# Kernel optimization log

Measured on AMD Instinct MI355X. Metric: run time of the kernel, lower is better.

Reference implementation:

```python
import jax, jax.numpy as jnp
from jax import lax
import numpy as np

EPS_BN = 1e-5


def _bn(x, g, b, axis):
    # eval-mode BatchNorm with running_mean=0, running_var=1
    shape = [1] * x.ndim
    shape[axis] = -1
    scale = (g / jnp.sqrt(1.0 + EPS_BN)).reshape(shape)
    return x * scale + b.reshape(shape)


def farthest_point_sample(xyz, npoint):
    B, N, _ = xyz.shape
    bidx = jnp.arange(B)

    def body(carry, _):
        dist, far = carry                      # [B,N], [B]
        centroid = xyz[bidx, far]              # [B,3]
        d = jnp.sum((xyz - centroid[:, None, :]) ** 2, axis=-1)
        dist = jnp.minimum(dist, d)
        return (dist, jnp.argmax(dist, axis=-1)), far

    init = (jnp.full((B, N), 1e10, xyz.dtype), jnp.zeros((B,), jnp.int32))
    _, idxs = lax.scan(body, init, None, length=npoint)
    return idxs.T                              # [B,npoint]


def square_distance(src, dst):
    # [B,S,3] x [B,N,3] -> [B,S,N]
    d = -2.0 * jnp.einsum('bsc,bnc->bsn', src, dst)
    d = d + jnp.sum(src ** 2, -1)[:, :, None] + jnp.sum(dst ** 2, -1)[:, None, :]
    return d


def sample_and_group(npoint, nsample, xyz, points):
    B = xyz.shape[0]
    bidx = jnp.arange(B)
    fps_idx = farthest_point_sample(xyz, npoint)          # [B,S]
    new_xyz = xyz[bidx[:, None], fps_idx]                 # [B,S,3]
    new_points = points[bidx[:, None], fps_idx]           # [B,S,C]
    dists = square_distance(new_xyz, xyz)                 # [B,S,N]
    _, idx = lax.top_k(-dists, nsample)                   # nearest nsample
    grouped = points[bidx[:, None, None], idx]            # [B,S,K,C]
    grouped_norm = grouped - new_points[:, :, None, :]
    rep = jnp.broadcast_to(new_points[:, :, None, :], grouped.shape)
    return new_xyz, jnp.concatenate([grouped_norm, rep], axis=-1)  # [B,S,K,2C]


def local_op(x, w, g, b):
    # x [B,S,K,D]; conv1d k=1 over channels D, BN, ReLU, max over K -> [B,out,S]
    y = jnp.einsum('bskd,od->bsko', x, w)
    y = jax.nn.relu(_bn(y, g, b, axis=3))
    y = jnp.max(y, axis=2)                                # [B,S,out]
    return jnp.transpose(y, (0, 2, 1))                    # [B,out,S]


def sa_layer(x, qk_w, v_w, v_b, t_w, t_b, g, b):
    # x [B,C,N]; q and k share weights (offset attention)
    xq = jnp.einsum('bcn,oc->bno', x, qk_w)               # [B,N,C/4]
    xk = jnp.einsum('bcn,oc->bon', x, qk_w)               # [B,C/4,N]
    xv = jnp.einsum('bcn,oc->bon', x, v_w) + v_b[:, None]
    energy = jnp.einsum('bnd,bdm->bnm', xq, xk)           # [B,N,N]
    attn = jax.nn.softmax(energy, axis=-1)
    attn = attn / (1e-9 + attn.sum(axis=1, keepdims=True))
    x_r = jnp.einsum('bcn,bnm->bcm', xv, attn)
    x_r = jnp.einsum('bcn,oc->bon', x - x_r, t_w) + t_b[:, None]
    x_r = jax.nn.relu(_bn(x_r, g, b, axis=1))
    return x + x_r


def setup_inputs() -> dict:
    key = jax.random.key(0)
    ks = iter(jax.random.split(key, 48))
    rn = lambda shape, s=0.05: jax.random.normal(next(ks), shape, jnp.float32) * s
    inp = {
        'xyz': jax.random.normal(next(ks), (32, 16384, 3), jnp.float32),
        'f': jax.random.normal(next(ks), (32, 16384, 3), jnp.float32),
        'conv1_w': rn((64, 6)), 'bn1_g': jnp.ones(64), 'bn1_b': jnp.zeros(64),
        'l0_w': rn((64, 128)), 'l0_g': jnp.ones(64), 'l0_b': jnp.zeros(64),
        'l1_w': rn((64, 128)), 'l1_g': jnp.ones(64), 'l1_b': jnp.zeros(64),
        'st_c1_w': rn((64, 64)), 'st_bn1_g': jnp.ones(64), 'st_bn1_b': jnp.zeros(64),
        'st_c2_w': rn((64, 64)), 'st_bn2_g': jnp.ones(64), 'st_bn2_b': jnp.zeros(64),
        'sa1_qk_w': rn((16, 64)), 'sa1_v_w': rn((64, 64)), 'sa1_v_b': jnp.zeros(64),
        'sa1_t_w': rn((64, 64)), 'sa1_t_b': jnp.zeros(64), 'sa1_g': jnp.ones(64), 'sa1_b': jnp.zeros(64),
        'sa2_qk_w': rn((16, 64)), 'sa2_v_w': rn((64, 64)), 'sa2_v_b': jnp.zeros(64),
        'sa2_t_w': rn((64, 64)), 'sa2_t_b': jnp.zeros(64), 'sa2_g': jnp.ones(64), 'sa2_b': jnp.zeros(64),
        'fuse_w': rn((256, 192)), 'fuse_g': jnp.ones(256), 'fuse_b': jnp.zeros(256),
        'lin1_w': rn((256, 256)), 'bn6_g': jnp.ones(256), 'bn6_b': jnp.zeros(256),
        'lin2_w': rn((256, 256)), 'lin2_b': jnp.zeros(256),
    }
    return inp


def _forward(xyz, f, conv1_w, bn1_g, bn1_b, l0_w, l0_g, l0_b, l1_w, l1_g, l1_b,
             st_c1_w, st_bn1_g, st_bn1_b, st_c2_w, st_bn2_g, st_bn2_b,
             sa1_qk_w, sa1_v_w, sa1_v_b, sa1_t_w, sa1_t_b, sa1_g, sa1_b,
             sa2_qk_w, sa2_v_w, sa2_v_b, sa2_t_w, sa2_t_b, sa2_g, sa2_b,
             fuse_w, fuse_g, fuse_b, lin1_w, bn6_g, bn6_b, lin2_w, lin2_b):
    center = jnp.mean(xyz, axis=1)                        # [B,3]
    xyz_c = xyz - center[:, None, :]
    pts = jnp.concatenate([xyz_c, f], axis=2)             # [B,N,6]
    geo = pts[..., :3]
    xin = jnp.transpose(pts, (0, 2, 1))                   # [B,6,N]
    x = jax.nn.relu(_bn(jnp.einsum('bcn,oc->bon', xin, conv1_w), bn1_g, bn1_b, 1))
    x = jnp.transpose(x, (0, 2, 1))                       # [B,N,64]
    new_xyz, nf = sample_and_group(128, 32, geo, x)
    feature_0 = local_op(nf, l0_w, l0_g, l0_b)            # [B,64,128]
    feature = jnp.transpose(feature_0, (0, 2, 1))
    _, nf2 = sample_and_group(32, 16, new_xyz, feature)
    feature_1 = local_op(nf2, l1_w, l1_g, l1_b)           # [B,64,32]
    # StackedAttention
    x = jax.nn.relu(_bn(jnp.einsum('bcn,oc->bon', feature_1, st_c1_w), st_bn1_g, st_bn1_b, 1))
    x = jax.nn.relu(_bn(jnp.einsum('bcn,oc->bon', x, st_c2_w), st_bn2_g, st_bn2_b, 1))
    x1 = sa_layer(x, sa1_qk_w, sa1_v_w, sa1_v_b, sa1_t_w, sa1_t_b, sa1_g, sa1_b)
    x2 = sa_layer(x1, sa2_qk_w, sa2_v_w, sa2_v_b, sa2_t_w, sa2_t_b, sa2_g, sa2_b)
    x = jnp.concatenate([x1, x2], axis=1)                 # [B,128,32]
    x = jnp.concatenate([x, feature_1], axis=1)           # [B,192,32]
    x = jax.nn.leaky_relu(_bn(jnp.einsum('bcn,oc->bon', x, fuse_w), fuse_g, fuse_b, 1), 0.2)
    x = jnp.max(x, axis=2)                                # [B,256]
    x = jax.nn.relu(_bn(x @ lin1_w.T, bn6_g, bn6_b, 1))   # dropout = identity (eval)
    x = x @ lin2_w.T + lin2_b
    return center, x


def reference(xyz, f, conv1_w, bn1_g, bn1_b, l0_w, l0_g, l0_b, l1_w, l1_g, l1_b,
              st_c1_w, st_bn1_g, st_bn1_b, st_c2_w, st_bn2_g, st_bn2_b,
              sa1_qk_w, sa1_v_w, sa1_v_b, sa1_t_w, sa1_t_b, sa1_g, sa1_b,
              sa2_qk_w, sa2_v_w, sa2_v_b, sa2_t_w, sa2_t_b, sa2_g, sa2_b,
              fuse_w, fuse_g, fuse_b, lin1_w, bn6_g, bn6_b, lin2_w, lin2_b):
    return _forward(xyz, f, conv1_w, bn1_g, bn1_b, l0_w, l0_g, l0_b, l1_w, l1_g, l1_b,
                    st_c1_w, st_bn1_g, st_bn1_b, st_c2_w, st_bn2_g, st_bn2_b,
                    sa1_qk_w, sa1_v_w, sa1_v_b, sa1_t_w, sa1_t_b, sa1_g, sa1_b,
                    sa2_qk_w, sa2_v_w, sa2_v_b, sa2_t_w, sa2_t_b, sa2_g, sa2_b,
                    fuse_w, fuse_g, fuse_b, lin1_w, bn6_g, bn6_b, lin2_w, lin2_b)
```

## Files before the change

### kernel.cpp

```cpp
#include <hip/hip_runtime.h>


__device__ __forceinline__ float bnscale(float g){ return g / sqrtf(1.0f + 1e-5f); }

__device__ __forceinline__ float conv_feat6(float p0,float p1,float p2,float p3,float p4,float p5,
                                            float w0,float w1,float w2,float w3,float w4,float w5,
                                            float sc,float bs){
    float y = p0*w0;
    y = fmaf(p1,w1,y); y = fmaf(p2,w2,y); y = fmaf(p3,w3,y);
    y = fmaf(p4,w4,y); y = fmaf(p5,w5,y);
    return fmaxf(fmaf(y,sc,bs), 0.0f);
}

__device__ __forceinline__ float fpsdist(float dx,float dy,float dz){
    #pragma clang fp contract(off)
    return (dx*dx + dy*dy) + dz*dz;
}

__device__ __forceinline__ float sumsq3(float x,float y,float z){
    #pragma clang fp contract(off)
    return (x*x + y*y) + z*z;
}
__device__ __forceinline__ float sqdist3(float qx,float qy,float qz,float qs,
                                         float px,float py,float pz){
    #pragma clang fp contract(off)
    {
        float dot = (qx*px + qy*py) + qz*pz;
        float pn  = (px*px + py*py) + pz*pz;
        return (-2.0f*dot + qs) + pn;
    }
}

__device__ __forceinline__ unsigned long long packdi(float d, unsigned int idx){
    unsigned int u = __float_as_uint(d);
    unsigned int msk = (unsigned int)((int)u >> 31);
    u ^= (msk | 0x80000000u);
    return ((unsigned long long)u << 32) | (unsigned long long)idx;
}

__device__ __forceinline__ unsigned long long u64min(unsigned long long a, unsigned long long b){
    return a < b ? a : b;
}

__device__ __forceinline__ unsigned long long u64_shfl_down(unsigned long long v, int off){
    unsigned int lo = (unsigned int)v, hi = (unsigned int)(v >> 32);
    lo = __shfl_down(lo, off, 64);
    hi = __shfl_down(hi, off, 64);
    return ((unsigned long long)hi << 32) | (unsigned long long)lo;
}

__device__ __forceinline__ unsigned long long u64_bcast0(unsigned long long v){
    unsigned int lo = (unsigned int)v, hi = (unsigned int)(v >> 32);
    lo = __shfl(lo, 0, 64);
    hi = __shfl(hi, 0, 64);
    return ((unsigned long long)hi << 32) | (unsigned long long)lo;
}

__global__ __launch_bounds__(512, 2) void k_fps1(const float* __restrict__ xyz,
                                                 float* __restrict__ center,
                                                 float* __restrict__ out,
                                                 int* __restrict__ idx_out){
    constexpr int NTH = 512, PPT = 32, N = 16384, NPOINT = 128, NW = 8;
    int b = blockIdx.x, t = threadIdx.x;
    int wid = t>>6, lane = t&63;

    __shared__ float s_red[NW][3];
    __shared__ unsigned int s_khi[2][NW], s_klo[2][NW];

    const float* xb = xyz + (size_t)b*N*3;
    float px[PPT], py[PPT], pz[PPT], dist[PPT];
    #pragma unroll
    for (int i=0;i<PPT;i++){
        const float* sp = xb + (size_t)(t + i*NTH)*3;
        px[i]=sp[0]; py[i]=sp[1]; pz[i]=sp[2];
        dist[i]=1e10f;
    }
    float sx=0.f, sy=0.f, sz=0.f;
    #pragma unroll
    for (int i=0;i<PPT;i++){ sx+=px[i]; sy+=py[i]; sz+=pz[i]; }
    #pragma unroll
    for (int off=32; off>=1; off>>=1){
        sx += __shfl_down(sx, off, 64);
        sy += __shfl_down(sy, off, 64);
        sz += __shfl_down(sz, off, 64);
    }
    if (lane==0){ s_red[wid][0]=sx; s_red[wid][1]=sy; s_red[wid][2]=sz; }
    __syncthreads();
    float cx0=0.f, cy0=0.f, cz0=0.f;
    #pragma unroll
    for (int w2=0; w2<NW; ++w2){ cx0+=s_red[w2][0]; cy0+=s_red[w2][1]; cz0+=s_red[w2][2]; }
    cx0 *= (1.0f/16384.0f); cy0 *= (1.0f/16384.0f); cz0 *= (1.0f/16384.0f);
    if (t < 3){
        float c = (t==0)?cx0:((t==1)?cy0:cz0);
        center[b*3+t] = c;
        out[b*3+t] = c;
    }
    #pragma unroll
    for (int i=0;i<PPT;i++){ px[i]-=cx0; py[i]-=cy0; pz[i]-=cz0; }
    if (t==0) idx_out[b*NPOINT] = 0;

    float cx = xb[0]-cx0, cy = xb[1]-cy0, cz = xb[2]-cz0;

    for (int it=1; it<NPOINT; ++it){
        int par = it & 1;
        float bv = -1.0f; int bi = 0;
        #pragma unroll
        for (int i=0;i<PPT;i++){
            float d = fpsdist(px[i]-cx, py[i]-cy, pz[i]-cz);
            float nd = fminf(dist[i], d);
            dist[i] = nd;
            bool better = nd > bv;
            bv = better ? nd : bv;
            bi = better ? (t + i*NTH) : bi;
        }
        unsigned long long key = ((unsigned long long)__float_as_uint(bv) << 32)
                               | (unsigned long long)(unsigned)(~(unsigned)bi);
        #pragma unroll
        for (int off=32; off>=1; off>>=1){
            unsigned long long ok = u64_shfl_down(key, off);
            key = ok > key ? ok : key;
        }
        if (lane==0){ s_khi[par][wid]=(unsigned)(key>>32); s_klo[par][wid]=(unsigned)key; }
        __syncthreads();
        unsigned long long gk = ((unsigned long long)s_khi[par][0] << 32) | s_klo[par][0];
        #pragma unroll
        for (int w2=1; w2<NW; ++w2){
            unsigned long long k2 = ((unsigned long long)s_khi[par][w2] << 32) | s_klo[par][w2];
            if (k2 > gk) gk = k2;
        }
        int gi = (int)(~(unsigned)(gk & 0xFFFFFFFFull));
        gi = __builtin_amdgcn_readfirstlane(gi);
        if (t==0) idx_out[b*NPOINT + it] = gi;
        const float* wp = xb + (size_t)gi*3;
        cx = wp[0]-cx0; cy = wp[1]-cy0; cz = wp[2]-cz0;
    }
}

__global__ __launch_bounds__(64) void k_fps2(const float* __restrict__ pts,
                                             int* __restrict__ idx_out){
    int b = blockIdx.x, lane = threadIdx.x;
    const float* pb = pts + (size_t)b*128*3;
    float px[2],py[2],pz[2],dist[2];
    #pragma unroll
    for (int i=0;i<2;i++){
        const float* sp = pb + (size_t)(lane + i*64)*3;
        px[i]=sp[0]; py[i]=sp[1]; pz[i]=sp[2];
        dist[i]=1e10f;
    }
    if (lane==0) idx_out[b*32] = 0;
    float cx=pb[0], cy=pb[1], cz=pb[2];

    for (int it=1; it<32; ++it){
        float bv=-1.0f; int bi=0;
        float bx=0.f, by=0.f, bz=0.f;
        #pragma unroll
        for (int i=0;i<2;i++){
            float d = fpsdist(px[i]-cx, py[i]-cy, pz[i]-cz);
            float nd = fminf(dist[i], d);
            dist[i]=nd;
            bool better = nd > bv;
            bv = better ? nd : bv;
            bi = better ? (lane + i*64) : bi;
            bx = better ? px[i] : bx;
            by = better ? py[i] : by;
            bz = better ? pz[i] : bz;
        }
        unsigned long long key = ((unsigned long long)__float_as_uint(bv) << 32)
                               | (unsigned long long)(unsigned)(~(unsigned)bi);
        #pragma unroll
        for (int off=32; off>=1; off>>=1){
            unsigned long long ok = u64_shfl_down(key, off);
            float ox = __shfl_down(bx, off, 64);
            float oy = __shfl_down(by, off, 64);
            float oz = __shfl_down(bz, off, 64);
            bool better = ok > key;
            key = better ? ok : key;
            bx = better ? ox : bx;
            by = better ? oy : by;
            bz = better ? oz : bz;
        }
        key = u64_bcast0(key);
        cx = __shfl(bx, 0, 64); cy = __shfl(by, 0, 64); cz = __shfl(bz, 0, 64);
        if (lane==0) idx_out[b*32 + it] = (int)(~(unsigned)(key & 0xFFFFFFFFull));
    }
}

__global__ __launch_bounds__(64) void k_gather1(const float* __restrict__ xyz,
                                                const float* __restrict__ f,
                                                const float* __restrict__ center,
                                                const float* __restrict__ conv1_w,
                                                const float* __restrict__ bn1_g,
                                                const float* __restrict__ bn1_b,
                                                const int* __restrict__ fps_idx,
                                                float* __restrict__ new_xyz,
                                                float* __restrict__ np_feat){
    int q = blockIdx.x; int b = q>>7, s = q&127;
    int o = threadIdx.x;
    int idx = fps_idx[b*128+s];
    const float* xp = xyz + ((size_t)b*16384 + idx)*3;
    const float* fp = f   + ((size_t)b*16384 + idx)*3;
    float p0 = xp[0]-center[b*3+0], p1 = xp[1]-center[b*3+1], p2 = xp[2]-center[b*3+2];
    float p3 = fp[0], p4 = fp[1], p5 = fp[2];
    const float* w = conv1_w + o*6;
    float v = conv_feat6(p0,p1,p2,p3,p4,p5, w[0],w[1],w[2],w[3],w[4],w[5],
                         bnscale(bn1_g[o]), bn1_b[o]);
    np_feat[((size_t)b*128 + s)*64 + o] = v;
    if (o < 3){
        float pc = (o==0)?p0:((o==1)?p1:p2);
        new_xyz[((size_t)b*128 + s)*3 + o] = pc;
    }
}

__global__ __launch_bounds__(256) void k_knn1(const float* __restrict__ xyz,
                                              const float* __restrict__ center,
                                              const float* __restrict__ new_xyz,
                                              int* __restrict__ knn_idx){
    int q = blockIdx.x; int b = q>>7;
    int t = threadIdx.x;
    __shared__ unsigned long long scmin[256];

    float cx = center[b*3+0], cy = center[b*3+1], cz = center[b*3+2];
    float qx = new_xyz[(size_t)q*3+0], qy = new_xyz[(size_t)q*3+1], qz = new_xyz[(size_t)q*3+2];
    float qs = sumsq3(qx,qy,qz);
    const float* xb = xyz + (size_t)b*16384*3;

    unsigned long long m = 0xFFFFFFFFFFFFFFFFull;
    for (int i=0;i<64;i++){
        int n = t + (i<<8);
        const float* p = xb + (size_t)n*3;
        float px = p[0]-cx, py = p[1]-cy, pz = p[2]-cz;
        float d = sqdist3(qx,qy,qz,qs,px,py,pz);
        m = u64min(m, packdi(d, (unsigned)n));
    }
    scmin[t] = m;
    __syncthreads();
    if (t >= 64) return;

    for (int r=0; r<32; ++r){
        unsigned long long mm = u64min(u64min(scmin[t], scmin[t+64]),
                                       u64min(scmin[t+128], scmin[t+192]));
        #pragma unroll
        for (int off=32; off>=1; off>>=1) mm = u64min(mm, u64_shfl_down(mm, off));
        unsigned long long win = u64_bcast0(mm);
        unsigned int widx = (unsigned int)(win & 0xFFFFFFFFull);
        if (t==0) knn_idx[(size_t)q*32 + r] = (int)widx;
        int c = (int)(widx & 255u);
        int n = c + (t<<8);
        const float* p = xb + (size_t)n*3;
        float px = p[0]-cx, py = p[1]-cy, pz = p[2]-cz;
        float d = sqdist3(qx,qy,qz,qs,px,py,pz);
        unsigned long long pk = packdi(d, (unsigned)n);
        if (pk <= win) pk = 0xFFFFFFFFFFFFFFFFull;
        #pragma unroll
        for (int off=32; off>=1; off>>=1) pk = u64min(pk, u64_shfl_down(pk, off));
        if (t==0) scmin[c] = pk;
    }
}

__global__ __launch_bounds__(64) void k_gather2(const float* __restrict__ new_xyz1,
                                                const float* __restrict__ feat,
                                                const int* __restrict__ fps2,
                                                float* __restrict__ new_xyz2,
                                                float* __restrict__ np2){
    int q = blockIdx.x; int b = q>>5, s = q&31;
    int o = threadIdx.x;
    int idx = fps2[b*32+s];
    np2[((size_t)b*32 + s)*64 + o] = feat[((size_t)b*128 + idx)*64 + o];
    if (o < 3) new_xyz2[((size_t)b*32 + s)*3 + o] = new_xyz1[((size_t)b*128 + idx)*3 + o];
}

__global__ __launch_bounds__(256) void k_knn2(const float* __restrict__ pts,
                                              const float* __restrict__ qpts,
                                              int* __restrict__ knn_idx){
    int t = threadIdx.x;
    int wid = t>>6, lane = t&63;
    int q = blockIdx.x*4 + wid;
    int b = q>>5;
    float qx = qpts[(size_t)q*3+0], qy = qpts[(size_t)q*3+1], qz = qpts[(size_t)q*3+2];
    float qs = sumsq3(qx,qy,qz);
    const float* pb = pts + (size_t)b*128*3;

    unsigned long long p0, p1;
    {
        int n = lane;
        float px=pb[n*3+0], py=pb[n*3+1], pz=pb[n*3+2];
        p0 = packdi(sqdist3(qx,qy,qz,qs,px,py,pz), (unsigned)n);
        n = lane + 64;
        px=pb[n*3+0]; py=pb[n*3+1]; pz=pb[n*3+2];
        p1 = packdi(sqdist3(qx,qy,qz,qs,px,py,pz), (unsigned)n);
    }
    for (int r=0; r<16; ++r){
        unsigned long long mm = u64min(p0, p1);
        #pragma unroll
        for (int off=32; off>=1; off>>=1) mm = u64min(mm, u64_shfl_down(mm, off));
        unsigned long long win = u64_bcast0(mm);
        if (lane==0) knn_idx[(size_t)q*16 + r] = (int)(win & 0xFFFFFFFFull);
        if (p0 == win) p0 = 0xFFFFFFFFFFFFFFFFull;
        if (p1 == win) p1 = 0xFFFFFFFFFFFFFFFFull;
    }
}

template<int K, int NQ, int NSRC, bool RECOMP>
__global__ __launch_bounds__(256, 2) void k_group_local(
    const float* __restrict__ xyz, const float* __restrict__ f, const float* __restrict__ center,
    const float* __restrict__ conv1_w, const float* __restrict__ bn1_g, const float* __restrict__ bn1_b,
    const float* __restrict__ src_feat,
    const int* __restrict__ knn_idx, const float* __restrict__ np_feat,
    const float* __restrict__ w, const float* __restrict__ g, const float* __restrict__ bb,
    float* __restrict__ out)
{
    __shared__ float wt[128*65];
    __shared__ float s_sc[64], s_bs[64];
    __shared__ float cwT[6*64];
    __shared__ float s_csc[64], s_cbs[64];
    __shared__ float np_l[4][64];
    __shared__ float gda[4][K][64];
    __shared__ float s_pts[4][K][6];

    int t = threadIdx.x;
    for (int e=t; e<8192; e+=256){ int o = e>>7, d = e&127; wt[d*65 + o] = w[e]; }
    if (t < 64){ s_sc[t] = bnscale(g[t]); s_bs[t] = bb[t]; }
    if constexpr (RECOMP){
        for (int e=t; e<384; e+=256){ int o = e/6, j = e%6; cwT[j*64 + o] = conv1_w[e]; }
        if (t < 64){ s_csc[t] = bnscale(bn1_g[t]); s_cbs[t] = bn1_b[t]; }
    }
    __syncthreads();

    int wid = t>>6, lane = t&63;
    int q = blockIdx.x*4 + wid;
    int b = q / NQ, s = q % NQ;

    float np_o = np_feat[((size_t)b*NQ + s)*64 + lane];
    np_l[wid][lane] = np_o;

    const int* kix = knn_idx + ((size_t)b*NQ + s)*K;

    if constexpr (RECOMP){
        float cx = center[b*3+0], cy = center[b*3+1], cz = center[b*3+2];
        if (lane < K){
            int myi = kix[lane];
            const float* xp = xyz + ((size_t)b*16384 + myi)*3;
            s_pts[wid][lane][0] = xp[0]-cx;
            s_pts[wid][lane][1] = xp[1]-cy;
            s_pts[wid][lane][2] = xp[2]-cz;
            const float* fp = f + ((size_t)b*16384 + myi)*3;
            s_pts[wid][lane][3] = fp[0];
            s_pts[wid][lane][4] = fp[1];
            s_pts[wid][lane][5] = fp[2];
        }
        #pragma unroll
        for (int k=0; k<K; ++k){
            float gv = conv_feat6(s_pts[wid][k][0], s_pts[wid][k][1], s_pts[wid][k][2],
                                  s_pts[wid][k][3], s_pts[wid][k][4], s_pts[wid][k][5],
                                  cwT[0*64+lane], cwT[1*64+lane], cwT[2*64+lane],
                                  cwT[3*64+lane], cwT[4*64+lane], cwT[5*64+lane],
                                  s_csc[lane], s_cbs[lane]);
            gda[wid][k][lane] = gv - np_o;
        }
    } else {
        int myi = kix[lane < K ? lane : 0];
        #pragma unroll
        for (int k=0; k<K; ++k){
            int ik = __shfl(myi, k, 64);
            gda[wid][k][lane] = src_feat[((size_t)b*NSRC + ik)*64 + lane] - np_o;
        }
    }

    float C = 0.f;
    #pragma unroll
    for (int d=0; d<64; d++) C = fmaf(np_l[wid][d], wt[(64+d)*65 + lane], C);

    float acc_y[K];
    #pragma unroll
    for (int k=0;k<K;k++) acc_y[k] = C;

    #pragma unroll
    for (int c=0; c<2; ++c){
        float wr[32];
        #pragma unroll
        for (int j=0;j<32;j++) wr[j] = wt[(c*32+j)*65 + lane];
        #pragma unroll
        for (int k=0;k<K;k++){
            const float4* g4 = (const float4*)&gda[wid][k][c*32];
            float yk = 0.f;
            #pragma unroll
            for (int j4=0;j4<8;j4++){
                float4 gg = g4[j4];
                yk = fmaf(gg.x, wr[j4*4+0], yk);
                yk = fmaf(gg.y, wr[j4*4+1], yk);
                yk = fmaf(gg.z, wr[j4*4+2], yk);
                yk = fmaf(gg.w, wr[j4*4+3], yk);
            }
            acc_y[k] = acc_y[k] + yk;
        }
    }

    float acc = -1e30f;
    #pragma unroll
    for (int k=0;k<K;k++){
        float v = fmaxf(fmaf(acc_y[k], s_sc[lane], s_bs[lane]), 0.0f);
        acc = fmaxf(acc, v);
    }
    out[((size_t)b*NQ + s)*64 + lane] = acc;
}

__device__ void sa_block(const float* X, float* Xout,
                         float* Q, float* E, float* XV, float* XR, float* CS,
                         const float* qk_w, const float* v_w, const float* v_b,
                         const float* t_w, const float* t_b,
                         const float* g, const float* bb, int t)
{
    for (int e=t; e<512; e+=256){
        int n = e>>4, o = e&15;
        float y = 0.f;
        for (int c=0;c<64;c++) y = fmaf(qk_w[o*64+c], X[c*32+n], y);
        Q[n*16+o] = y;
    }
    for (int e=t; e<2048; e+=256){
        int o = e>>5, n = e&31;
        float y = v_b[o];
        for (int c=0;c<64;c++) y = fmaf(v_w[o*64+c], X[c*32+n], y);
        XV[o*32+n] = y;
    }
    __syncthreads();
    for (int e=t; e<1024; e+=256){
        int n = e>>5, m = e&31;
        float y = 0.f;
        for (int d=0;d<16;d++) y = fmaf(Q[n*16+d], Q[m*16+d], y);
        E[e] = y;
    }
    __syncthreads();
    if (t < 32){
        float mx = -1e30f;
        for (int m=0;m<32;m++) mx = fmaxf(mx, E[t*32+m]);
        float sum = 0.f;
        for (int m=0;m<32;m++){ float v = expf(E[t*32+m]-mx); E[t*32+m]=v; sum += v; }
        for (int m=0;m<32;m++) E[t*32+m] = E[t*32+m] / sum;
    }
    __syncthreads();
    if (t < 32){
        float cs = 0.f;
        for (int n=0;n<32;n++) cs += E[n*32+t];
        CS[t] = 1e-9f + cs;
    }
    __syncthreads();
    for (int e=t; e<1024; e+=256) E[e] = E[e] / CS[e&31];
    __syncthreads();
    for (int e=t; e<2048; e+=256){
        int c = e>>5, m = e&31;
        float y = 0.f;
        for (int n=0;n<32;n++) y = fmaf(XV[c*32+n], E[n*32+m], y);
        XR[c*32+m] = y;
    }
    __syncthreads();
    for (int e=t; e<2048; e+=256){
        int o = e>>5, n = e&31;
        float y = 0.f;
        for (int c=0;c<64;c++) y = fmaf(t_w[o*64+c], X[c*32+n]-XR[c*32+n], y);
        y += t_b[o];
        y = fmaxf(fmaf(y, bnscale(g[o]), bb[o]), 0.0f);
        Xout[e] = X[e] + y;
    }
    __syncthreads();
}

__global__ __launch_bounds__(256) void k_tail(
    const float* __restrict__ f1buf,
    const float* st_c1_w, const float* st_bn1_g, const float* st_bn1_b,
    const float* st_c2_w, const float* st_bn2_g, const float* st_bn2_b,
    const float* sa1_qk, const float* sa1_v, const float* sa1_vb,
    const float* sa1_t, const float* sa1_tb, const float* sa1_g, const float* sa1_b,
    const float* sa2_qk, const float* sa2_v, const float* sa2_vb,
    const float* sa2_t, const float* sa2_tb, const float* sa2_g, const float* sa2_b,
    const float* fuse_w, const float* fuse_g, const float* fuse_b,
    const float* lin1_w, const float* bn6_g, const float* bn6_b,
    const float* lin2_w, const float* lin2_b,
    float* __restrict__ out)
{
    __shared__ float sm[14848];
    float* F1 = sm;
    float* XA = sm + 2048;
    float* XB = sm + 4096;
    float* Q  = sm + 6144;
    float* E  = sm + 6656;
    float* XV = sm + 7680;
    float* XR = sm + 9728;
    float* CS = sm + 11776;
    float* FO = sm + 6144;
    float* PO = sm + 14336;
    float* P2 = sm + 14592;

    int b = blockIdx.x, t = threadIdx.x;

    for (int e=t; e<2048; e+=256){ int n = e>>6, c = e&63; F1[c*32+n] = f1buf[((size_t)b*32+n)*64 + c]; }
    __syncthreads();
    for (int e=t; e<2048; e+=256){
        int o = e>>5, n = e&31;
        float y = 0.f;
        for (int c=0;c<64;c++) y = fmaf(st_c1_w[o*64+c], F1[c*32+n], y);
        XA[e] = fmaxf(fmaf(y, bnscale(st_bn1_g[o]), st_bn1_b[o]), 0.0f);
    }
    __syncthreads();
    for (int e=t; e<2048; e+=256){
        int o = e>>5, n = e&31;
        float y = 0.f;
        for (int c=0;c<64;c++) y = fmaf(st_c2_w[o*64+c], XA[c*32+n], y);
        XB[e] = fmaxf(fmaf(y, bnscale(st_bn2_g[o]), st_bn2_b[o]), 0.0f);
    }
    __syncthreads();
    sa_block(XB, XA, Q,E,XV,XR,CS, sa1_qk, sa1_v, sa1_vb, sa1_t, sa1_tb, sa1_g, sa1_b, t);
    sa_block(XA, XB, Q,E,XV,XR,CS, sa2_qk, sa2_v, sa2_vb, sa2_t, sa2_tb, sa2_g, sa2_b, t);
    for (int e=t; e<8192; e+=256){
        int o = e>>5, n = e&31;
        const float* wr = fuse_w + o*192;
        float y = 0.f;
        for (int c=0;c<64;c++) y = fmaf(wr[c],      XA[c*32+n], y);
        for (int c=0;c<64;c++) y = fmaf(wr[64+c],   XB[c*32+n], y);
        for (int c=0;c<64;c++) y = fmaf(wr[128+c],  F1[c*32+n], y);
        float v = fmaf(y, bnscale(fuse_g[o]), fuse_b[o]);
        FO[e] = (v > 0.0f) ? v : 0.2f*v;
    }
    __syncthreads();
    {
        float mx = -1e30f;
        for (int n=0;n<32;n++) mx = fmaxf(mx, FO[t*32+n]);
        PO[t] = mx;
    }
    __syncthreads();
    {
        const float* wr = lin1_w + t*256;
        float y = 0.f;
        for (int c=0;c<256;c++) y = fmaf(wr[c], PO[c], y);
        P2[t] = fmaxf(fmaf(y, bnscale(bn6_g[t]), bn6_b[t]), 0.0f);
    }
    __syncthreads();
    {
        const float* wr = lin2_w + t*256;
        float y = 0.f;
        for (int c=0;c<256;c++) y = fmaf(wr[c], P2[c], y);
        out[96 + b*256 + t] = y + lin2_b[t];
    }
}

extern "C" void kernel_launch(void* const* d_in, const int* in_sizes, int n_in,
                              void* d_out, int out_size, void* d_ws, size_t ws_size,
                              hipStream_t stream)
{
    const float* xyz      = (const float*)d_in[0];
    const float* f        = (const float*)d_in[1];
    const float* conv1_w  = (const float*)d_in[2];
    const float* bn1_g    = (const float*)d_in[3];
    const float* bn1_b    = (const float*)d_in[4];
    const float* l0_w     = (const float*)d_in[5];
    const float* l0_g     = (const float*)d_in[6];
    const float* l0_b     = (const float*)d_in[7];
    const float* l1_w     = (const float*)d_in[8];
    const float* l1_g     = (const float*)d_in[9];
    const float* l1_b     = (const float*)d_in[10];
    const float* st_c1_w  = (const float*)d_in[11];
    const float* st_bn1_g = (const float*)d_in[12];
    const float* st_bn1_b = (const float*)d_in[13];
    const float* st_c2_w  = (const float*)d_in[14];
    const float* st_bn2_g = (const float*)d_in[15];
    const float* st_bn2_b = (const float*)d_in[16];
    const float* sa1_qk   = (const float*)d_in[17];
    const float* sa1_v    = (const float*)d_in[18];
    const float* sa1_vb   = (const float*)d_in[19];
    const float* sa1_t    = (const float*)d_in[20];
    const float* sa1_tb   = (const float*)d_in[21];
    const float* sa1_g    = (const float*)d_in[22];
    const float* sa1_b    = (const float*)d_in[23];
    const float* sa2_qk   = (const float*)d_in[24];
    const float* sa2_v    = (const float*)d_in[25];
    const float* sa2_vb   = (const float*)d_in[26];
    const float* sa2_t    = (const float*)d_in[27];
    const float* sa2_tb   = (const float*)d_in[28];
    const float* sa2_g    = (const float*)d_in[29];
    const float* sa2_b    = (const float*)d_in[30];
    const float* fuse_w   = (const float*)d_in[31];
    const float* fuse_g   = (const float*)d_in[32];
    const float* fuse_b   = (const float*)d_in[33];
    const float* lin1_w   = (const float*)d_in[34];
    const float* bn6_g    = (const float*)d_in[35];
    const float* bn6_b    = (const float*)d_in[36];
    const float* lin2_w   = (const float*)d_in[37];
    const float* lin2_b   = (const float*)d_in[38];
    float* out = (float*)d_out;

    float* ws = (float*)d_ws;
    float* center   = ws + 0;
    float* new_xyz1 = ws + 96;
    float* np1      = ws + 12384;
    float* feat     = ws + 274528;
    float* new_xyz2 = ws + 536672;
    float* np2      = ws + 539744;
    float* f1       = ws + 605280;
    int*   fps1     = (int*)(ws + 670816);
    int*   knn1     = (int*)(ws + 674912);
    int*   fps2     = (int*)(ws + 805984);
    int*   knn2     = (int*)(ws + 807008);

    k_fps1<<<32, 512, 0, stream>>>(xyz, center, out, fps1);
    k_gather1<<<4096, 64, 0, stream>>>(xyz, f, center, conv1_w, bn1_g, bn1_b, fps1, new_xyz1, np1);
    k_knn1<<<4096, 256, 0, stream>>>(xyz, center, new_xyz1, knn1);
    k_group_local<32,128,1,true><<<1024, 256, 0, stream>>>(
        xyz, f, center, conv1_w, bn1_g, bn1_b, nullptr, knn1, np1, l0_w, l0_g, l0_b, feat);
    k_fps2<<<32, 64, 0, stream>>>(new_xyz1, fps2);
    k_gather2<<<1024, 64, 0, stream>>>(new_xyz1, feat, fps2, new_xyz2, np2);
    k_knn2<<<256, 256, 0, stream>>>(new_xyz1, new_xyz2, knn2);
    k_group_local<16,32,128,false><<<256, 256, 0, stream>>>(
        nullptr, nullptr, nullptr, nullptr, nullptr, nullptr, feat, knn2, np2, l1_w, l1_g, l1_b, f1);
    k_tail<<<32, 256, 0, stream>>>(f1,
        st_c1_w, st_bn1_g, st_bn1_b, st_c2_w, st_bn2_g, st_bn2_b,
        sa1_qk, sa1_v, sa1_vb, sa1_t, sa1_tb, sa1_g, sa1_b,
        sa2_qk, sa2_v, sa2_vb, sa2_t, sa2_tb, sa2_g, sa2_b,
        fuse_w, fuse_g, fuse_b, lin1_w, bn6_g, bn6_b, lin2_w, lin2_b, out);
}
```

Measured before the change: 651.9 us.

## Fuse gather into KNN1 and merge stage-two FPS/KNN/grouping into tail kernel

Folds the first gather into the KNN1 kernel, which now runs one query per wavefront with register-held per-lane minima instead of a shared-memory array, and launches four times fewer blocks. Stage-two FPS, gather, KNN and grouped local conv are all moved into the tail kernel, one block per batch, so intermediate buffers and several launches go away. FPS1 tracks the slot index rather than the global index and relaxes launch bounds to one block per CU. The cost is a much larger shared-memory footprint and serialised work inside only 32 blocks for the stage-two part.

```diff
diff --git a/kernel.cpp b/kernel.cpp
--- a/kernel.cpp
+++ b/kernel.cpp
@@ -56,7 +56,7 @@
     return ((unsigned long long)hi << 32) | (unsigned long long)lo;
 }
 
-__global__ __launch_bounds__(512, 2) void k_fps1(const float* __restrict__ xyz,
+__global__ __launch_bounds__(512, 1) void k_fps1(const float* __restrict__ xyz,
                                                  float* __restrict__ center,
                                                  float* __restrict__ out,
                                                  int* __restrict__ idx_out){
@@ -103,16 +103,17 @@
 
     for (int it=1; it<NPOINT; ++it){
         int par = it & 1;
-        float bv = -1.0f; int bi = 0;
+        float bv = -1.0f; int bis = 0;
         #pragma unroll
         for (int i=0;i<PPT;i++){
             float d = fpsdist(px[i]-cx, py[i]-cy, pz[i]-cz);
             float nd = fminf(dist[i], d);
             dist[i] = nd;
             bool better = nd > bv;
-            bv = better ? nd : bv;
-            bi = better ? (t + i*NTH) : bi;
-        }
+            bv  = better ? nd : bv;
+            bis = better ? i  : bis;
+        }
+        int bi = t + (bis<<9);
         unsigned long long key = ((unsigned long long)__float_as_uint(bv) << 32)
                                | (unsigned long long)(unsigned)(~(unsigned)bi);
         #pragma unroll
@@ -136,167 +137,83 @@
     }
 }
 
-__global__ __launch_bounds__(64) void k_fps2(const float* __restrict__ pts,
-                                             int* __restrict__ idx_out){
-    int b = blockIdx.x, lane = threadIdx.x;
-    const float* pb = pts + (size_t)b*128*3;
-    float px[2],py[2],pz[2],dist[2];
-    #pragma unroll
-    for (int i=0;i<2;i++){
-        const float* sp = pb + (size_t)(lane + i*64)*3;
-        px[i]=sp[0]; py[i]=sp[1]; pz[i]=sp[2];
-        dist[i]=1e10f;
-    }
-    if (lane==0) idx_out[b*32] = 0;
-    float cx=pb[0], cy=pb[1], cz=pb[2];
-
-    for (int it=1; it<32; ++it){
-        float bv=-1.0f; int bi=0;
-        float bx=0.f, by=0.f, bz=0.f;
-        #pragma unroll
-        for (int i=0;i<2;i++){
-            float d = fpsdist(px[i]-cx, py[i]-cy, pz[i]-cz);
-            float nd = fminf(dist[i], d);
-            dist[i]=nd;
-            bool better = nd > bv;
-            bv = better ? nd : bv;
-            bi = better ? (lane + i*64) : bi;
-            bx = better ? px[i] : bx;
-            by = better ? py[i] : by;
-            bz = better ? pz[i] : bz;
-        }
-        unsigned long long key = ((unsigned long long)__float_as_uint(bv) << 32)
-                               | (unsigned long long)(unsigned)(~(unsigned)bi);
-        #pragma unroll
-        for (int off=32; off>=1; off>>=1){
-            unsigned long long ok = u64_shfl_down(key, off);
-            float ox = __shfl_down(bx, off, 64);
-            float oy = __shfl_down(by, off, 64);
-            float oz = __shfl_down(bz, off, 64);
-            bool better = ok > key;
-            key = better ? ok : key;
-            bx = better ? ox : bx;
-            by = better ? oy : by;
-            bz = better ? oz : bz;
-        }
-        key = u64_bcast0(key);
-        cx = __shfl(bx, 0, 64); cy = __shfl(by, 0, 64); cz = __shfl(bz, 0, 64);
-        if (lane==0) idx_out[b*32 + it] = (int)(~(unsigned)(key & 0xFFFFFFFFull));
-    }
-}
-
-__global__ __launch_bounds__(64) void k_gather1(const float* __restrict__ xyz,
-                                                const float* __restrict__ f,
-                                                const float* __restrict__ center,
-                                                const float* __restrict__ conv1_w,
-                                                const float* __restrict__ bn1_g,
-                                                const float* __restrict__ bn1_b,
-                                                const int* __restrict__ fps_idx,
-                                                float* __restrict__ new_xyz,
-                                                float* __restrict__ np_feat){
-    int q = blockIdx.x; int b = q>>7, s = q&127;
-    int o = threadIdx.x;
+__global__ __launch_bounds__(256) void k_knn1(const float* __restrict__ xyz,
+                                              const float* __restrict__ f,
+                                              const float* __restrict__ center,
+                                              const float* __restrict__ conv1_w,
+                                              const float* __restrict__ bn1_g,
+                                              const float* __restrict__ bn1_b,
+                                              const int* __restrict__ fps_idx,
+                                              float* __restrict__ new_xyz,
+                                              float* __restrict__ np_feat,
+                                              int* __restrict__ knn_idx){
+    int t = threadIdx.x, wid = t>>6, lane = t&63;
+    int q = blockIdx.x*4 + wid;
+    int b = q>>7, s = q&127;
+
+    float cx = center[b*3+0], cy = center[b*3+1], cz = center[b*3+2];
     int idx = fps_idx[b*128+s];
     const float* xp = xyz + ((size_t)b*16384 + idx)*3;
     const float* fp = f   + ((size_t)b*16384 + idx)*3;
-    float p0 = xp[0]-center[b*3+0], p1 = xp[1]-center[b*3+1], p2 = xp[2]-center[b*3+2];
+    float p0 = xp[0]-cx, p1 = xp[1]-cy, p2 = xp[2]-cz;
     float p3 = fp[0], p4 = fp[1], p5 = fp[2];
-    const float* w = conv1_w + o*6;
-    float v = conv_feat6(p0,p1,p2,p3,p4,p5, w[0],w[1],w[2],w[3],w[4],w[5],
-                         bnscale(bn1_g[o]), bn1_b[o]);
-    np_feat[((size_t)b*128 + s)*64 + o] = v;
-    if (o < 3){
-        float pc = (o==0)?p0:((o==1)?p1:p2);
-        new_xyz[((size_t)b*128 + s)*3 + o] = pc;
-    }
-}
-
-__global__ __launch_bounds__(256) void k_knn1(const float* __restrict__ xyz,
-                                              const float* __restrict__ center,
-                                              const float* __restrict__ new_xyz,
-                                              int* __restrict__ knn_idx){
-    int q = blockIdx.x; int b = q>>7;
-    int t = threadIdx.x;
-    __shared__ unsigned long long scmin[256];
-
-    float cx = center[b*3+0], cy = center[b*3+1], cz = center[b*3+2];
-    float qx = new_xyz[(size_t)q*3+0], qy = new_xyz[(size_t)q*3+1], qz = new_xyz[(size_t)q*3+2];
+
+    {
+        const float* w6 = conv1_w + lane*6;
+        float v = conv_feat6(p0,p1,p2,p3,p4,p5, w6[0],w6[1],w6[2],w6[3],w6[4],w6[5],
+                             bnscale(bn1_g[lane]), bn1_b[lane]);
+        np_feat[(size_t)q*64 + lane] = v;
+        if (lane < 3){
+            float pc = (lane==0)?p0:((lane==1)?p1:p2);
+            new_xyz[(size_t)q*3 + lane] = pc;
+        }
+    }
+
+    float qx = p0, qy = p1, qz = p2;
     float qs = sumsq3(qx,qy,qz);
     const float* xb = xyz + (size_t)b*16384*3;
 
-    unsigned long long m = 0xFFFFFFFFFFFFFFFFull;
-    for (int i=0;i<64;i++){
-        int n = t + (i<<8);
-        const float* p = xb + (size_t)n*3;
-        float px = p[0]-cx, py = p[1]-cy, pz = p[2]-cz;
-        float d = sqdist3(qx,qy,qz,qs,px,py,pz);
-        m = u64min(m, packdi(d, (unsigned)n));
-    }
-    scmin[t] = m;
-    __syncthreads();
-    if (t >= 64) return;
-
+    unsigned long long m0=~0ull, m1=~0ull, m2=~0ull, m3=~0ull;
+    for (int i=0; i<256; i+=4){
+        #pragma unroll
+        for (int j=0;j<4;j++){
+            int n = lane + ((i+j)<<6);
+            const float* p = xb + (size_t)n*3;
+            float dx = p[0]-cx, dy = p[1]-cy, dz = p[2]-cz;
+            float d = sqdist3(qx,qy,qz,qs,dx,dy,dz);
+            unsigned long long pk = packdi(d,(unsigned)n);
+            if (j==0) m0 = u64min(m0,pk);
+            else if (j==1) m1 = u64min(m1,pk);
+            else if (j==2) m2 = u64min(m2,pk);
+            else m3 = u64min(m3,pk);
+        }
+    }
+
+    size_t kbase = (size_t)q*32;
     for (int r=0; r<32; ++r){
-        unsigned long long mm = u64min(u64min(scmin[t], scmin[t+64]),
-                                       u64min(scmin[t+128], scmin[t+192]));
+        unsigned long long mm = u64min(u64min(m0,m1), u64min(m2,m3));
         #pragma unroll
         for (int off=32; off>=1; off>>=1) mm = u64min(mm, u64_shfl_down(mm, off));
         unsigned long long win = u64_bcast0(mm);
         unsigned int widx = (unsigned int)(win & 0xFFFFFFFFull);
-        if (t==0) knn_idx[(size_t)q*32 + r] = (int)widx;
+        if (lane==0) knn_idx[kbase + r] = (int)widx;
         int c = (int)(widx & 255u);
-        int n = c + (t<<8);
-        const float* p = xb + (size_t)n*3;
-        float px = p[0]-cx, py = p[1]-cy, pz = p[2]-cz;
-        float d = sqdist3(qx,qy,qz,qs,px,py,pz);
-        unsigned long long pk = packdi(d, (unsigned)n);
-        if (pk <= win) pk = 0xFFFFFFFFFFFFFFFFull;
+        int n2 = c + (lane<<8);
+        const float* p = xb + (size_t)n2*3;
+        float dx = p[0]-cx, dy = p[1]-cy, dz = p[2]-cz;
+        float d = sqdist3(qx,qy,qz,qs,dx,dy,dz);
+        unsigned long long pk = packdi(d,(unsigned)n2);
+        if (pk <= win) pk = ~0ull;
         #pragma unroll
         for (int off=32; off>=1; off>>=1) pk = u64min(pk, u64_shfl_down(pk, off));
-        if (t==0) scmin[c] = pk;
-    }
-}
-
-__global__ __launch_bounds__(64) void k_gather2(const float* __restrict__ new_xyz1,
-                                                const float* __restrict__ feat,
-                                                const int* __restrict__ fps2,
-                                                float* __restrict__ new_xyz2,
-                                                float* __restrict__ np2){
-    int q = blockIdx.x; int b = q>>5, s = q&31;
-    int o = threadIdx.x;
-    int idx = fps2[b*32+s];
-    np2[((size_t)b*32 + s)*64 + o] = feat[((size_t)b*128 + idx)*64 + o];
-    if (o < 3) new_xyz2[((size_t)b*32 + s)*3 + o] = new_xyz1[((size_t)b*128 + idx)*3 + o];
-}
-
-__global__ __launch_bounds__(256) void k_knn2(const float* __restrict__ pts,
-                                              const float* __restrict__ qpts,
-                                              int* __restrict__ knn_idx){
-    int t = threadIdx.x;
-    int wid = t>>6, lane = t&63;
-    int q = blockIdx.x*4 + wid;
-    int b = q>>5;
-    float qx = qpts[(size_t)q*3+0], qy = qpts[(size_t)q*3+1], qz = qpts[(size_t)q*3+2];
-    float qs = sumsq3(qx,qy,qz);
-    const float* pb = pts + (size_t)b*128*3;
-
-    unsigned long long p0, p1;
-    {
-        int n = lane;
-        float px=pb[n*3+0], py=pb[n*3+1], pz=pb[n*3+2];
-        p0 = packdi(sqdist3(qx,qy,qz,qs,px,py,pz), (unsigned)n);
-        n = lane + 64;
-        px=pb[n*3+0]; py=pb[n*3+1]; pz=pb[n*3+2];
-        p1 = packdi(sqdist3(qx,qy,qz,qs,px,py,pz), (unsigned)n);
-    }
-    for (int r=0; r<16; ++r){
-        unsigned long long mm = u64min(p0, p1);
-        #pragma unroll
-        for (int off=32; off>=1; off>>=1) mm = u64min(mm, u64_shfl_down(mm, off));
-        unsigned long long win = u64_bcast0(mm);
-        if (lane==0) knn_idx[(size_t)q*16 + r] = (int)(win & 0xFFFFFFFFull);
-        if (p0 == win) p0 = 0xFFFFFFFFFFFFFFFFull;
-        if (p1 == win) p1 = 0xFFFFFFFFFFFFFFFFull;
+        unsigned long long nm = u64_bcast0(pk);
+        int owner = c & 63, slot = c >> 6;
+        if (lane == owner){
+            if (slot==0) m0 = nm;
+            else if (slot==1) m1 = nm;
+            else if (slot==2) m2 = nm;
+            else m3 = nm;
+        }
     }
 }
 
@@ -464,8 +381,10 @@
     __syncthreads();
 }
 
-__global__ __launch_bounds__(256) void k_tail(
-    const float* __restrict__ f1buf,
+__global__ __launch_bounds__(256) void k_mega(
+    const float* __restrict__ new_xyz1,
+    const float* __restrict__ feat,
+    const float* __restrict__ l1_w, const float* __restrict__ l1_g, const float* __restrict__ l1_b,
     const float* st_c1_w, const float* st_bn1_g, const float* st_bn1_b,
     const float* st_c2_w, const float* st_bn2_g, const float* st_bn2_b,
     const float* sa1_qk, const float* sa1_v, const float* sa1_vb,
@@ -477,23 +396,160 @@
     const float* lin2_w, const float* lin2_b,
     float* __restrict__ out)
 {
-    __shared__ float sm[14848];
-    float* F1 = sm;
-    float* XA = sm + 2048;
-    float* XB = sm + 4096;
-    float* Q  = sm + 6144;
-    float* E  = sm + 6656;
-    float* XV = sm + 7680;
-    float* XR = sm + 9728;
-    float* CS = sm + 11776;
-    float* FO = sm + 6144;
-    float* PO = sm + 14336;
-    float* P2 = sm + 14592;
-
-    int b = blockIdx.x, t = threadIdx.x;
-
-    for (int e=t; e<2048; e+=256){ int n = e>>6, c = e&63; F1[c*32+n] = f1buf[((size_t)b*32+n)*64 + c]; }
-    __syncthreads();
+    __shared__ float nx1[384];
+    __shared__ int   s_i2[32];
+    __shared__ float np2L[2048];
+    __shared__ float nx2[96];
+    __shared__ int   s_k2[512];
+    __shared__ float wt[8320];
+    __shared__ float s_sc[64], s_bs[64];
+    __shared__ float gdaL[4][16][64];
+    __shared__ float smt[14848];
+
+    int b = blockIdx.x, t = threadIdx.x, wid = t>>6, lane = t&63;
+
+    for (int e=t; e<384; e+=256) nx1[e] = new_xyz1[(size_t)b*384 + e];
+    for (int e=t; e<8192; e+=256){ int o = e>>7, d = e&127; wt[d*65 + o] = l1_w[e]; }
+    if (t < 64){ s_sc[t] = bnscale(l1_g[t]); s_bs[t] = l1_b[t]; }
+    __syncthreads();
+
+    if (wid == 0){
+        float px[2],py[2],pz[2],dist[2];
+        #pragma unroll
+        for (int i=0;i<2;i++){
+            int n = lane + i*64;
+            px[i]=nx1[n*3+0]; py[i]=nx1[n*3+1]; pz[i]=nx1[n*3+2];
+            dist[i]=1e10f;
+        }
+        if (lane==0) s_i2[0] = 0;
+        float cx=nx1[0], cy=nx1[1], cz=nx1[2];
+        for (int it=1; it<32; ++it){
+            float bv=-1.0f; int bi=0;
+            float bx=0.f, by=0.f, bz=0.f;
+            #pragma unroll
+            for (int i=0;i<2;i++){
+                float d = fpsdist(px[i]-cx, py[i]-cy, pz[i]-cz);
+                float nd = fminf(dist[i], d);
+                dist[i]=nd;
+                bool better = nd > bv;
+                bv = better ? nd : bv;
+                bi = better ? (lane + i*64) : bi;
+                bx = better ? px[i] : bx;
+                by = better ? py[i] : by;
+                bz = better ? pz[i] : bz;
+            }
+            unsigned long long key = ((unsigned long long)__float_as_uint(bv) << 32)
+                                   | (unsigned long long)(unsigned)(~(unsigned)bi);
+            #pragma unroll
+            for (int off=32; off>=1; off>>=1){
+                unsigned long long ok = u64_shfl_down(key, off);
+                float ox = __shfl_down(bx, off, 64);
+                float oy = __shfl_down(by, off, 64);
+                float oz = __shfl_down(bz, off, 64);
+                bool better = ok > key;
+                key = better ? ok : key;
+                bx = better ? ox : bx;
+                by = better ? oy : by;
+                bz = better ? oz : bz;
+            }
+            key = u64_bcast0(key);
+            cx = __shfl(bx, 0, 64); cy = __shfl(by, 0, 64); cz = __shfl(bz, 0, 64);
+            if (lane==0) s_i2[it] = (int)(~(unsigned)(key & 0xFFFFFFFFull));
+        }
+    }
+    __syncthreads();
+
+    for (int e=t; e<2048; e+=256){
+        int s = e>>6, o = e&63;
+        np2L[s*64 + o] = feat[((size_t)b*128 + s_i2[s])*64 + o];
+    }
+    if (t < 32){
+        int idx = s_i2[t];
+        nx2[t*3+0] = nx1[idx*3+0];
+        nx2[t*3+1] = nx1[idx*3+1];
+        nx2[t*3+2] = nx1[idx*3+2];
+    }
+    __syncthreads();
+
+    for (int j=0;j<8;j++){
+        int s = wid + 4*j;
+        float qx = nx2[s*3+0], qy = nx2[s*3+1], qz = nx2[s*3+2];
+        float qs = sumsq3(qx,qy,qz);
+        unsigned long long pp0, pp1;
+        {
+            float ax=nx1[lane*3+0], ay=nx1[lane*3+1], az=nx1[lane*3+2];
+            pp0 = packdi(sqdist3(qx,qy,qz,qs,ax,ay,az), (unsigned)lane);
+            ax=nx1[(lane+64)*3+0]; ay=nx1[(lane+64)*3+1]; az=nx1[(lane+64)*3+2];
+            pp1 = packdi(sqdist3(qx,qy,qz,qs,ax,ay,az), (unsigned)(lane+64));
+        }
+        for (int r=0; r<16; ++r){
+            unsigned long long mm = u64min(pp0, pp1);
+            #pragma unroll
+            for (int off=32; off>=1; off>>=1) mm = u64min(mm, u64_shfl_down(mm, off));
+            unsigned long long win = u64_bcast0(mm);
+            if (lane==0) s_k2[s*16 + r] = (int)(win & 0xFFFFFFFFull);
+            if (pp0 == win) pp0 = ~0ull;
+            if (pp1 == win) pp1 = ~0ull;
+        }
+    }
+    __syncthreads();
+
+    for (int j=0;j<8;j++){
+        int s = wid + 4*j;
+        float np_o = np2L[s*64 + lane];
+        #pragma unroll
+        for (int k=0;k<16;k++){
+            int ik = s_k2[s*16 + k];
+            gdaL[wid][k][lane] = feat[((size_t)b*128 + ik)*64 + lane] - np_o;
+        }
+        float C0 = 0.f;
+        #pragma unroll
+        for (int d=0; d<64; d++) C0 = fmaf(np2L[s*64 + d], wt[(64+d)*65 + lane], C0);
+        float acc_y[16];
+        #pragma unroll
+        for (int k=0;k<16;k++) acc_y[k] = C0;
+        #pragma unroll
+        for (int c=0; c<2; ++c){
+            float wr[32];
+            #pragma unroll
+            for (int jj=0;jj<32;jj++) wr[jj] = wt[(c*32+jj)*65 + lane];
+            #pragma unroll
+            for (int k=0;k<16;k++){
+                const float4* g4 = (const float4*)&gdaL[wid][k][c*32];
+                float yk = 0.f;
+                #pragma unroll
+                for (int j4=0;j4<8;j4++){
+                    float4 gg = g4[j4];
+                    yk = fmaf(gg.x, wr[j4*4+0], yk);
+                    yk = fmaf(gg.y, wr[j4*4+1], yk);
+                    yk = fmaf(gg.z, wr[j4*4+2], yk);
+                    yk = fmaf(gg.w, wr[j4*4+3], yk);
+                }
+                acc_y[k] = acc_y[k] + yk;
+            }
+        }
+        float acc = -1e30f;
+        #pragma unroll
+        for (int k=0;k<16;k++){
+            float v = fmaxf(fmaf(acc_y[k], s_sc[lane], s_bs[lane]), 0.0f);
+            acc = fmaxf(acc, v);
+        }
+        smt[lane*32 + s] = acc;
+    }
+    __syncthreads();
+
+    float* F1 = smt;
+    float* XA = smt + 2048;
+    float* XB = smt + 4096;
+    float* Q  = smt + 6144;
+    float* E  = smt + 6656;
+    float* XV = smt + 7680;
+    float* XR = smt + 9728;
+    float* CS = smt + 11776;
+    float* FO = smt + 6144;
+    float* PO = smt + 14336;
+    float* P2 = smt + 14592;
+
     for (int e=t; e<2048; e+=256){
         int o = e>>5, n = e&31;
         float y = 0.f;
@@ -592,25 +648,16 @@
     float* new_xyz1 = ws + 96;
     float* np1      = ws + 12384;
     float* feat     = ws + 274528;
-    float* new_xyz2 = ws + 536672;
-    float* np2      = ws + 539744;
-    float* f1       = ws + 605280;
-    int*   fps1     = (int*)(ws + 670816);
-    int*   knn1     = (int*)(ws + 674912);
-    int*   fps2     = (int*)(ws + 805984);
-    int*   knn2     = (int*)(ws + 807008);
+    int*   fps1     = (int*)(ws + 536672);
+    int*   knn1     = (int*)(ws + 540768);
 
     k_fps1<<<32, 512, 0, stream>>>(xyz, center, out, fps1);
-    k_gather1<<<4096, 64, 0, stream>>>(xyz, f, center, conv1_w, bn1_g, bn1_b, fps1, new_xyz1, np1);
-    k_knn1<<<4096, 256, 0, stream>>>(xyz, center, new_xyz1, knn1);
+    k_knn1<<<1024, 256, 0, stream>>>(xyz, f, center, conv1_w, bn1_g, bn1_b,
+                                     fps1, new_xyz1, np1, knn1);
     k_group_local<32,128,1,true><<<1024, 256, 0, stream>>>(
         xyz, f, center, conv1_w, bn1_g, bn1_b, nullptr, knn1, np1, l0_w, l0_g, l0_b, feat);
-    k_fps2<<<32, 64, 0, stream>>>(new_xyz1, fps2);
-    k_gather2<<<1024, 64, 0, stream>>>(new_xyz1, feat, fps2, new_xyz2, np2);
-    k_knn2<<<256, 256, 0, stream>>>(new_xyz1, new_xyz2, knn2);
-    k_group_local<16,32,128,false><<<256, 256, 0, stream>>>(
-        nullptr, nullptr, nullptr, nullptr, nullptr, nullptr, feat, knn2, np2, l1_w, l1_g, l1_b, f1);
-    k_tail<<<32, 256, 0, stream>>>(f1,
+    k_mega<<<32, 256, 0, stream>>>(new_xyz1, feat,
+        l1_w, l1_g, l1_b,
         st_c1_w, st_bn1_g, st_bn1_b, st_c2_w, st_bn2_g, st_bn2_b,
         sa1_qk, sa1_v, sa1_vb, sa1_t, sa1_tb, sa1_g, sa1_b,
         sa2_qk, sa2_v, sa2_vb, sa2_t, sa2_tb, sa2_g, sa2_b,
```

Result: slower. 729.5 us (+11.9%).
